# Kernel optimization log

Hardware: AMD Instinct MI355X
Metric: run time of the kernel (lower is better)

The kernel has to match this reference:

```python
import jax, jax.numpy as jnp
import numpy as np

B, N, D, H = 4, 2048, 768, 12
DK = D // H  # 64

def setup_inputs() -> dict:
    key = jax.random.key(0)
    ks = jax.random.split(key, 7)
    f = lambda k, shape: jax.random.normal(k, shape, dtype=jnp.float32)
    return {
        "Q": f(ks[0], (B, N, D)),
        "K": f(ks[1], (B, N, D)),
        "V": f(ks[2], (B, N, D)),
        "w_q": f(ks[3], (D, D)) * 0.02,
        "w_k": f(ks[4], (D, D)) * 0.02,
        "w_v": f(ks[5], (D, D)) * 0.02,
        "w_o": f(ks[6], (D, D)) * 0.02,
    }

def reference(Q, K, V, w_q, w_k, w_v, w_o):
    # Linear with bias=False: y = x @ W.T, W is [out, in]
    def proj(x, w):
        # [B, N, D] -> [B, H, N, DK]
        y = jnp.einsum('bnd,ed->bne', x, w)
        return y.reshape(B, N, H, DK).transpose(0, 2, 1, 3)
    q = proj(Q, w_q)
    k = proj(K, w_k)
    v = proj(V, w_v)
    scale = 1.0 / jnp.sqrt(jnp.float32(DK))
    scores = jnp.einsum('bhqd,bhkd->bhqk', q, k) * scale  # [B,H,N,N]
    weights = jax.nn.softmax(scores, axis=-1)
    out = jnp.einsum('bhqk,bhkd->bhqd', weights, v)  # [B,H,N,DK]
    out = out.transpose(0, 2, 1, 3).reshape(B, N, D)
    return jnp.einsum('bnd,ed->bne', out, w_o)
```

## Files before the change

kernel.cpp:

```cpp
#include <hip/hip_runtime.h>

typedef unsigned short ushortT;
typedef __attribute__((ext_vector_type(8))) short bf16x8;
typedef __attribute__((ext_vector_type(4))) float f32x4;
typedef __attribute__((ext_vector_type(16))) float f32x16;
typedef __attribute__((ext_vector_type(2))) int i32x2;

#define QSCALE 0.18033688011112042f

__device__ __forceinline__ unsigned short f2bf(float f) {
  unsigned int u = __float_as_uint(f);
  u += 0x7FFFu + ((u >> 16) & 1u);
  return (unsigned short)(u >> 16);
}
__device__ __forceinline__ unsigned short f2bf_fast(float f) {
  unsigned int u = __float_as_uint(f) + 0x8000u;
  return (unsigned short)(u >> 16);
}

__device__ __forceinline__ void gl16(const void* g, void* l) {
  __builtin_amdgcn_global_load_lds(
      (const __attribute__((address_space(1))) void*)g,
      (__attribute__((address_space(3))) void*)l, 16, 0, 0);
}

__device__ __forceinline__ unsigned cvtpk(float lo, float hi) {
  unsigned r;
  asm("v_cvt_pk_bf16_f32 %0, %1, %2" : "=v"(r) : "v"(lo), "v"(hi));
  return r;
}

__global__ __launch_bounds__(256) void cvt_all(
    const float* __restrict__ q, const float* __restrict__ k, const float* __restrict__ v,
    const float* __restrict__ w0, const float* __restrict__ w1,
    const float* __restrict__ w2, const float* __restrict__ w3,
    ushortT* xq, ushortT* xk, ushortT* xv,
    ushortT* bw0, ushortT* bw1, ushortT* bw2, ushortT* bw3) {
  int t = blockIdx.y;
  const float* src; ushortT* dst; int n;
  switch (t) {
    case 0: src = q;  dst = xq;  n = 8192 * 768; break;
    case 1: src = k;  dst = xk;  n = 8192 * 768; break;
    case 2: src = v;  dst = xv;  n = 8192 * 768; break;
    case 3: src = w0; dst = bw0; n = 768 * 768;  break;
    case 4: src = w1; dst = bw1; n = 768 * 768;  break;
    case 5: src = w2; dst = bw2; n = 768 * 768;  break;
    default: src = w3; dst = bw3; n = 768 * 768; break;
  }
  int i = (blockIdx.x * 256 + threadIdx.x) * 4;
  if (i >= n) return;
  float4 f = *(const float4*)(src + i);
  ushort4 o = make_ushort4(f2bf(f.x), f2bf(f.y), f2bf(f.z), f2bf(f.w));
  *(ushort4*)(dst + i) = o;
}

__global__ __launch_bounds__(256) void gemm_qkv(
    const ushortT* __restrict__ xq, const ushortT* __restrict__ xk,
    const ushortT* __restrict__ xv, const ushortT* __restrict__ bwq,
    const ushortT* __restrict__ bwk, const ushortT* __restrict__ bwv,
    ushortT* qp, ushortT* kp, ushortT* vtp) {
  constexpr int K = 768;
  __shared__ __attribute__((aligned(16))) ushortT As[128 * 32];
  __shared__ __attribute__((aligned(16))) ushortT Bs[128 * 32];
  const int tid = threadIdx.x;
  const int w = tid >> 6, l = tid & 63;
  const int z = blockIdx.z, bx = blockIdx.x;
  const ushortT* A;
  const ushortT* Bm;
  int m0, n0;
  if (z < 2) {
    A = z ? xk : xq; Bm = z ? bwk : bwq;
    m0 = (bx / 6) * 128; n0 = (bx % 6) * 128;
  } else {
    A = bwv; Bm = xv;
    m0 = (bx % 6) * 128; n0 = (bx / 6) * 128;
  }
  const ushortT* Ab = A  + (size_t)m0 * K;
  const ushortT* Bb = Bm + (size_t)n0 * K;

  f32x4 acc[4][4] = {};
  const int wr = w >> 1, wc = w & 1;
  const int lg = l >> 4, li = l & 15;
  const int srow = tid >> 2, scol = (tid & 3) * 8;

  for (int k0 = 0; k0 < K; k0 += 32) {
    gl16(Ab + (size_t)srow * K + (k0 + scol),        &As[w * 512]);
    gl16(Ab + (size_t)(64 + srow) * K + (k0 + scol), &As[2048 + w * 512]);
    gl16(Bb + (size_t)srow * K + (k0 + scol),        &Bs[w * 512]);
    gl16(Bb + (size_t)(64 + srow) * K + (k0 + scol), &Bs[2048 + w * 512]);
    __syncthreads();
    bf16x8 af[4], bfr[4];
#pragma unroll
    for (int mi = 0; mi < 4; ++mi)
      af[mi] = *(const bf16x8*)&As[(wr * 64 + mi * 16 + li) * 32 + lg * 8];
#pragma unroll
    for (int ni = 0; ni < 4; ++ni)
      bfr[ni] = *(const bf16x8*)&Bs[(wc * 64 + ni * 16 + li) * 32 + lg * 8];
#pragma unroll
    for (int mi = 0; mi < 4; ++mi)
#pragma unroll
      for (int ni = 0; ni < 4; ++ni)
        acc[mi][ni] = __builtin_amdgcn_mfma_f32_16x16x32_bf16(af[mi], bfr[ni], acc[mi][ni], 0, 0, 0);
    __syncthreads();
  }

  const float sc = (z == 0) ? QSCALE : 1.0f;
  ushortT* dst0 = (z == 0) ? qp : kp;
#pragma unroll
  for (int mi = 0; mi < 4; ++mi) {
#pragma unroll
    for (int ni = 0; ni < 4; ++ni) {
#pragma unroll
      for (int r = 0; r < 4; ++r) {
        int m = m0 + wr * 64 + mi * 16 + lg * 4 + r;
        int n = n0 + wc * 64 + ni * 16 + li;
        float val = acc[mi][ni][r];
        if (z < 2) {
          int b = m >> 11, nn = m & 2047, hh = n >> 6, dk = n & 63;
          dst0[(((size_t)(b * 12 + hh)) * 2048 + nn) * 64 + dk] = f2bf_fast(val * sc);
        } else {
          vtp[(size_t)m * 8192 + n] = f2bf_fast(val);
        }
      }
    }
  }
}

__global__ __launch_bounds__(256) void gemm_out(
    const ushortT* __restrict__ A0, const ushortT* __restrict__ B0, float* O0) {
  constexpr int K = 768;
  __shared__ __attribute__((aligned(16))) ushortT As[128 * 32];
  __shared__ __attribute__((aligned(16))) ushortT Bs[128 * 32];
  const int tid = threadIdx.x;
  const int w = tid >> 6, l = tid & 63;
  const int m0 = blockIdx.y * 128, n0 = blockIdx.x * 128;
  const ushortT* Ab = A0 + (size_t)m0 * K;
  const ushortT* Bb = B0 + (size_t)n0 * K;

  f32x4 acc[4][4] = {};
  const int wr = w >> 1, wc = w & 1;
  const int lg = l >> 4, li = l & 15;
  const int srow = tid >> 2, scol = (tid & 3) * 8;

  for (int k0 = 0; k0 < K; k0 += 32) {
    gl16(Ab + (size_t)srow * K + (k0 + scol),        &As[w * 512]);
    gl16(Ab + (size_t)(64 + srow) * K + (k0 + scol), &As[2048 + w * 512]);
    gl16(Bb + (size_t)srow * K + (k0 + scol),        &Bs[w * 512]);
    gl16(Bb + (size_t)(64 + srow) * K + (k0 + scol), &Bs[2048 + w * 512]);
    __syncthreads();
    bf16x8 af[4], bfr[4];
#pragma unroll
    for (int mi = 0; mi < 4; ++mi)
      af[mi] = *(const bf16x8*)&As[(wr * 64 + mi * 16 + li) * 32 + lg * 8];
#pragma unroll
    for (int ni = 0; ni < 4; ++ni)
      bfr[ni] = *(const bf16x8*)&Bs[(wc * 64 + ni * 16 + li) * 32 + lg * 8];
#pragma unroll
    for (int mi = 0; mi < 4; ++mi)
#pragma unroll
      for (int ni = 0; ni < 4; ++ni)
        acc[mi][ni] = __builtin_amdgcn_mfma_f32_16x16x32_bf16(af[mi], bfr[ni], acc[mi][ni], 0, 0, 0);
    __syncthreads();
  }

#pragma unroll
  for (int mi = 0; mi < 4; ++mi)
#pragma unroll
    for (int ni = 0; ni < 4; ++ni)
#pragma unroll
      for (int r = 0; r < 4; ++r) {
        int m = m0 + wr * 64 + mi * 16 + lg * 4 + r;
        int n = n0 + wc * 64 + ni * 16 + li;
        O0[(size_t)m * 768 + n] = acc[mi][ni][r];
      }
}

__global__ __launch_bounds__(256, 3) void attn(
    const ushortT* __restrict__ qp, const ushortT* __restrict__ kp,
    const ushortT* __restrict__ vtp, ushortT* __restrict__ ao) {
  __shared__ __attribute__((aligned(16))) ushortT Ks[128 * 64];
  __shared__ __attribute__((aligned(16))) ushortT Vs[2 * 64 * 64];
  __shared__ __attribute__((aligned(16))) ushortT Ot[4][32 * 72];
  const int tid = threadIdx.x;
  const int w = tid >> 6, l = tid & 63;
  const int lq = l & 31, h = l >> 5;

  const int flat = blockIdx.y * 16 + blockIdx.x;
  const int head = (flat & 7) * 6 + (flat >> 7);
  const int qt = (flat >> 3) & 15;
  const int bb = head / 12, hh = head % 12;
  const size_t hb = (size_t)head * 2048 * 64;
  const int q0 = qt * 128 + w * 32;

  const ushortT* kbase = kp + hb;
  const ushortT* vbase = vtp + (size_t)(hh * 64) * 8192 + (size_t)bb * 2048;

  const int srow8 = l >> 3;
  const int scol = ((l & 7) ^ srow8) << 3;

#define STAGE(kt)                                                              \
  {                                                                            \
    _Pragma("unroll") for (int j = 0; j < 4; ++j) {                            \
      int rk = (w << 5) + (j << 3) + srow8;                                    \
      gl16(kbase + (size_t)((kt) * 128 + rk) * 64 + scol,                      \
           (char*)Ks + ((w << 5) + (j << 3)) * 128);                           \
      int rv = ((w & 1) << 5) + (j << 3) + srow8;                              \
      gl16(vbase + (size_t)rv * 8192 + (kt) * 128 + (w >> 1) * 64 + scol,      \
           (char*)Vs + (w >> 1) * 8192 + (((w & 1) << 5) + (j << 3)) * 128);   \
    }                                                                          \
  }

  bf16x8 bq[4];
#pragma unroll
  for (int c = 0; c < 4; ++c)
    bq[c] = *(const bf16x8*)&qp[hb + (size_t)(q0 + lq) * 64 + c * 16 + h * 8];

  bf16x8 ones;
#pragma unroll
  for (int e = 0; e < 8; ++e) ones[e] = (short)0x3F80;

  f32x16 oa0 = {}, oa1 = {};
  f32x16 asum = {};
  const int lq7 = lq & 7;

  for (int kt = 0; kt < 16; ++kt) {
    STAGE(kt);
    __syncthreads();

#pragma unroll
    for (int khalf = 0; khalf < 2; ++khalf) {
      const char* kbuf = (const char*)Ks + khalf * 8192;
      const char* vbuf = (const char*)Vs + khalf * 8192;

      f32x16 s0 = {}, s1 = {};
      __builtin_amdgcn_s_setprio(1);
#pragma unroll
      for (int c = 0; c < 4; ++c) {
        bf16x8 a0 = *(const bf16x8*)(kbuf + lq * 128 + (((2 * c + h) ^ lq7) << 4));
        s0 = __builtin_amdgcn_mfma_f32_32x32x16_bf16(a0, bq[c], s0, 0, 0, 0);
      }
#pragma unroll
      for (int c = 0; c < 4; ++c) {
        bf16x8 a1 = *(const bf16x8*)(kbuf + (32 + lq) * 128 + (((2 * c + h) ^ lq7) << 4));
        s1 = __builtin_amdgcn_mfma_f32_32x32x16_bf16(a1, bq[c], s1, 0, 0, 0);
      }
      __builtin_amdgcn_s_setprio(0);

#pragma unroll
      for (int r = 0; r < 16; ++r) s0[r] = exp2f(s0[r]);
#pragma unroll
      for (int r = 0; r < 16; ++r) s1[r] = exp2f(s1[r]);

      unsigned c8[16];
#pragma unroll
      for (int n = 0; n < 8; ++n) c8[n]     = cvtpk(s0[2 * n], s0[2 * n + 1]);
#pragma unroll
      for (int n = 0; n < 8; ++n) c8[8 + n] = cvtpk(s1[2 * n], s1[2 * n + 1]);

      __builtin_amdgcn_s_setprio(1);
#pragma unroll
      for (int kcg = 0; kcg < 4; ++kcg) {
        const unsigned* cc = &c8[(kcg >> 1) * 8 + (kcg & 1) * 4];
        i32x2 rA = __builtin_amdgcn_permlane32_swap((int)cc[0], (int)cc[2], false, false);
        i32x2 rB = __builtin_amdgcn_permlane32_swap((int)cc[1], (int)cc[3], false, false);
        union { int u4[4]; bf16x8 v8; } pb;
        pb.u4[0] = rA[0]; pb.u4[1] = rB[0]; pb.u4[2] = rA[1]; pb.u4[3] = rB[1];
        bf16x8 av0 = *(const bf16x8*)(vbuf + lq * 128 + (((2 * kcg + h) ^ lq7) << 4));
        bf16x8 av1 = *(const bf16x8*)(vbuf + (32 + lq) * 128 + (((2 * kcg + h) ^ lq7) << 4));
        oa0 = __builtin_amdgcn_mfma_f32_32x32x16_bf16(av0, pb.v8, oa0, 0, 0, 0);
        oa1 = __builtin_amdgcn_mfma_f32_32x32x16_bf16(av1, pb.v8, oa1, 0, 0, 0);
        asum = __builtin_amdgcn_mfma_f32_32x32x16_bf16(ones, pb.v8, asum, 0, 0, 0);
      }
      __builtin_amdgcn_s_setprio(0);
    }

    __syncthreads();
  }
#undef STAGE

  ushortT* ot = Ot[w];
  float inv = 1.f / asum[0];
#pragma unroll
  for (int r4 = 0; r4 < 4; ++r4) {
    int d = 8 * r4 + 4 * h;
    uint2 p0, p1;
    p0.x = cvtpk(oa0[4 * r4 + 0] * inv, oa0[4 * r4 + 1] * inv);
    p0.y = cvtpk(oa0[4 * r4 + 2] * inv, oa0[4 * r4 + 3] * inv);
    p1.x = cvtpk(oa1[4 * r4 + 0] * inv, oa1[4 * r4 + 1] * inv);
    p1.y = cvtpk(oa1[4 * r4 + 2] * inv, oa1[4 * r4 + 3] * inv);
    *(uint2*)&ot[lq * 72 + d]      = p0;
    *(uint2*)&ot[lq * 72 + 32 + d] = p1;
  }
  asm volatile("s_waitcnt lgkmcnt(0)" ::: "memory");
  __builtin_amdgcn_sched_barrier(0);
  const int tq = l >> 1, dh = (l & 1) * 32;
  const size_t orow = ((size_t)(bb * 2048 + q0 + tq)) * 768 + hh * 64 + dh;
#pragma unroll
  for (int c = 0; c < 4; ++c) {
    bf16x8 x = *(const bf16x8*)&ot[tq * 72 + dh + c * 8];
    *(bf16x8*)&ao[orow + c * 8] = x;
  }
}

extern "C" void kernel_launch(void* const* d_in, const int* in_sizes, int n_in,
                              void* d_out, int out_size, void* d_ws, size_t ws_size,
                              hipStream_t stream) {
  const float* Q  = (const float*)d_in[0];
  const float* K_ = (const float*)d_in[1];
  const float* V  = (const float*)d_in[2];
  const float* wq = (const float*)d_in[3];
  const float* wk = (const float*)d_in[4];
  const float* wv = (const float*)d_in[5];
  const float* wo = (const float*)d_in[6];

  ushortT* xq  = (ushortT*)d_ws;
  ushortT* xk  = xq  + (size_t)8192 * 768;
  ushortT* xv  = xk  + (size_t)8192 * 768;
  ushortT* bwq = xv  + (size_t)8192 * 768;
  ushortT* bwk = bwq + (size_t)768 * 768;
  ushortT* bwv = bwk + (size_t)768 * 768;
  ushortT* bwo = bwv + (size_t)768 * 768;
  ushortT* qp  = bwo + (size_t)768 * 768;
  ushortT* kp  = qp  + (size_t)8192 * 768;
  ushortT* vtp = kp  + (size_t)8192 * 768;
  ushortT* aob = vtp + (size_t)8192 * 768;

  cvt_all<<<dim3(6144, 7), 256, 0, stream>>>(Q, K_, V, wq, wk, wv, wo,
                                             xq, xk, xv, bwq, bwk, bwv, bwo);

  gemm_qkv<<<dim3(384, 1, 3), 256, 0, stream>>>(xq, xk, xv, bwq, bwk, bwv,
                                                qp, kp, vtp);

  attn<<<dim3(16, 48), 256, 0, stream>>>(qp, kp, vtp, aob);

  gemm_out<<<dim3(6, 64), 256, 0, stream>>>(aob, bwo, (float*)d_out);
}
```

Baseline: 177.9 us.

## Fuse fp32-to-bf16 activation conversion into QKV projection GEMM loads

Removes the separate conversion pass over the Q/K/V activations. The QKV GEMM now reads fp32 activations directly, converts them in registers with packed bf16 conversion, and stores them to LDS, while the weights are still loaded with async global-to-LDS copies. Only the weights are pre-converted by a smaller kernel. This cuts a full write and re-read of the bf16 activation copies, but the GEMM now does synchronous register loads with twice the bytes per element and conversion ALU work before each barrier.

```diff
diff --git a/kernel.cpp b/kernel.cpp
--- a/kernel.cpp
+++ b/kernel.cpp
@@ -30,34 +30,29 @@
   return r;
 }
 
-__global__ __launch_bounds__(256) void cvt_all(
-    const float* __restrict__ q, const float* __restrict__ k, const float* __restrict__ v,
+__global__ __launch_bounds__(256) void cvt_w(
     const float* __restrict__ w0, const float* __restrict__ w1,
     const float* __restrict__ w2, const float* __restrict__ w3,
-    ushortT* xq, ushortT* xk, ushortT* xv,
     ushortT* bw0, ushortT* bw1, ushortT* bw2, ushortT* bw3) {
   int t = blockIdx.y;
-  const float* src; ushortT* dst; int n;
+  const float* src; ushortT* dst;
   switch (t) {
-    case 0: src = q;  dst = xq;  n = 8192 * 768; break;
-    case 1: src = k;  dst = xk;  n = 8192 * 768; break;
-    case 2: src = v;  dst = xv;  n = 8192 * 768; break;
-    case 3: src = w0; dst = bw0; n = 768 * 768;  break;
-    case 4: src = w1; dst = bw1; n = 768 * 768;  break;
-    case 5: src = w2; dst = bw2; n = 768 * 768;  break;
-    default: src = w3; dst = bw3; n = 768 * 768; break;
+    case 0: src = w0; dst = bw0; break;
+    case 1: src = w1; dst = bw1; break;
+    case 2: src = w2; dst = bw2; break;
+    default: src = w3; dst = bw3; break;
   }
   int i = (blockIdx.x * 256 + threadIdx.x) * 4;
-  if (i >= n) return;
   float4 f = *(const float4*)(src + i);
   ushort4 o = make_ushort4(f2bf(f.x), f2bf(f.y), f2bf(f.z), f2bf(f.w));
   *(ushort4*)(dst + i) = o;
 }
 
 __global__ __launch_bounds__(256) void gemm_qkv(
-    const ushortT* __restrict__ xq, const ushortT* __restrict__ xk,
-    const ushortT* __restrict__ xv, const ushortT* __restrict__ bwq,
-    const ushortT* __restrict__ bwk, const ushortT* __restrict__ bwv,
+    const float* __restrict__ fxq, const float* __restrict__ fxk,
+    const float* __restrict__ fxv,
+    const ushortT* __restrict__ bwq, const ushortT* __restrict__ bwk,
+    const ushortT* __restrict__ bwv,
     ushortT* qp, ushortT* kp, ushortT* vtp) {
   constexpr int K = 768;
   __shared__ __attribute__((aligned(16))) ushortT As[128 * 32];
@@ -65,18 +60,15 @@
   const int tid = threadIdx.x;
   const int w = tid >> 6, l = tid & 63;
   const int z = blockIdx.z, bx = blockIdx.x;
-  const ushortT* A;
-  const ushortT* Bm;
+  const float*   Fx = (z == 0) ? fxq : (z == 1 ? fxk : fxv);
+  const ushortT* Wb = (z == 0) ? bwq : (z == 1 ? bwk : bwv);
   int m0, n0;
-  if (z < 2) {
-    A = z ? xk : xq; Bm = z ? bwk : bwq;
-    m0 = (bx / 6) * 128; n0 = (bx % 6) * 128;
-  } else {
-    A = bwv; Bm = xv;
-    m0 = (bx % 6) * 128; n0 = (bx / 6) * 128;
-  }
-  const ushortT* Ab = A  + (size_t)m0 * K;
-  const ushortT* Bb = Bm + (size_t)n0 * K;
+  if (z < 2) { m0 = (bx / 6) * 128; n0 = (bx % 6) * 128; }
+  else       { m0 = (bx % 6) * 128; n0 = (bx / 6) * 128; }
+  const float*   Fb = Fx + (size_t)(z < 2 ? m0 : n0) * K;
+  const ushortT* Gb = Wb + (size_t)(z < 2 ? n0 : m0) * K;
+  ushortT* Fl = (z < 2) ? As : Bs;
+  ushortT* Gl = (z < 2) ? Bs : As;
 
   f32x4 acc[4][4] = {};
   const int wr = w >> 1, wc = w & 1;
@@ -84,10 +76,21 @@
   const int srow = tid >> 2, scol = (tid & 3) * 8;
 
   for (int k0 = 0; k0 < K; k0 += 32) {
-    gl16(Ab + (size_t)srow * K + (k0 + scol),        &As[w * 512]);
-    gl16(Ab + (size_t)(64 + srow) * K + (k0 + scol), &As[2048 + w * 512]);
-    gl16(Bb + (size_t)srow * K + (k0 + scol),        &Bs[w * 512]);
-    gl16(Bb + (size_t)(64 + srow) * K + (k0 + scol), &Bs[2048 + w * 512]);
+    const float* p0 = Fb + (size_t)srow * K + k0 + scol;
+    const float* p1 = Fb + (size_t)(64 + srow) * K + k0 + scol;
+    float4 a0 = *(const float4*)p0;
+    float4 a1 = *(const float4*)(p0 + 4);
+    float4 b0 = *(const float4*)p1;
+    float4 b1 = *(const float4*)(p1 + 4);
+    gl16(Gb + (size_t)srow * K + (k0 + scol),        (char*)Gl + w * 1024);
+    gl16(Gb + (size_t)(64 + srow) * K + (k0 + scol), (char*)Gl + 4096 + w * 1024);
+    union { unsigned u[4]; bf16x8 v; } pa, pb;
+    pa.u[0] = cvtpk(a0.x, a0.y); pa.u[1] = cvtpk(a0.z, a0.w);
+    pa.u[2] = cvtpk(a1.x, a1.y); pa.u[3] = cvtpk(a1.z, a1.w);
+    pb.u[0] = cvtpk(b0.x, b0.y); pb.u[1] = cvtpk(b0.z, b0.w);
+    pb.u[2] = cvtpk(b1.x, b1.y); pb.u[3] = cvtpk(b1.z, b1.w);
+    *(bf16x8*)&Fl[srow * 32 + scol]        = pa.v;
+    *(bf16x8*)&Fl[(64 + srow) * 32 + scol] = pb.v;
     __syncthreads();
     bf16x8 af[4], bfr[4];
 #pragma unroll
@@ -313,10 +316,7 @@
   const float* wv = (const float*)d_in[5];
   const float* wo = (const float*)d_in[6];
 
-  ushortT* xq  = (ushortT*)d_ws;
-  ushortT* xk  = xq  + (size_t)8192 * 768;
-  ushortT* xv  = xk  + (size_t)8192 * 768;
-  ushortT* bwq = xv  + (size_t)8192 * 768;
+  ushortT* bwq = (ushortT*)d_ws;
   ushortT* bwk = bwq + (size_t)768 * 768;
   ushortT* bwv = bwk + (size_t)768 * 768;
   ushortT* bwo = bwv + (size_t)768 * 768;
@@ -325,10 +325,9 @@
   ushortT* vtp = kp  + (size_t)8192 * 768;
   ushortT* aob = vtp + (size_t)8192 * 768;
 
-  cvt_all<<<dim3(6144, 7), 256, 0, stream>>>(Q, K_, V, wq, wk, wv, wo,
-                                             xq, xk, xv, bwq, bwk, bwv, bwo);
-
-  gemm_qkv<<<dim3(384, 1, 3), 256, 0, stream>>>(xq, xk, xv, bwq, bwk, bwv,
+  cvt_w<<<dim3(576, 4), 256, 0, stream>>>(wq, wk, wv, wo, bwq, bwk, bwv, bwo);
+
+  gemm_qkv<<<dim3(384, 1, 3), 256, 0, stream>>>(Q, K_, V, bwq, bwk, bwv,
                                                 qp, kp, vtp);
 
   attn<<<dim3(16, 48), 256, 0, stream>>>(qp, kp, vtp, aob);
```

Result: slower. 184.7 us (+3.8%).
